# Kernel tuning notes

Hardware: AMD Instinct MI355X
Metric: run time of the kernel (lower is better)

The kernel has to match this reference:

```python
import jax, jax.numpy as jnp
import numpy as np

W_MAE, W_GRAD, W_TV, W_BG, W_MSE = 1.0, 0.1, 0.002, 0.15, 1.0
EPS = 1e-8


def setup_inputs() -> dict:
    key = jax.random.key(0)
    k1, k2, k3 = jax.random.split(key, 3)
    B, C, D, H, W = 2, 3, 128, 128, 128
    pred = jax.random.normal(k1, (B, C, D, H, W), dtype=jnp.float32)
    target = jax.random.normal(k2, (B, C, D, H, W), dtype=jnp.float32)
    # binary foreground mask, broadcast over channels
    mask = (jax.random.uniform(k3, (B, 1, D, H, W)) > 0.5).astype(jnp.float32)
    return {"pred": pred, "target": target, "mask": mask}


def _grad3(x):
    dx = x[:, :, 1:, :, :] - x[:, :, :-1, :, :]
    dy = x[:, :, :, 1:, :] - x[:, :, :, :-1, :]
    dz = x[:, :, :, :, 1:] - x[:, :, :, :, :-1]
    return dx, dy, dz


def reference(pred, target, mask):
    C = pred.shape[1]

    def masked_mean(x, m):
        return (x * m).sum() / (m.sum() * C + EPS)

    pred_in = pred * mask
    tgt_in = target * mask
    diff = pred_in - tgt_in

    l_mae = masked_mean(jnp.abs(diff), mask)

    px, py, pz = _grad3(pred_in)
    tx, ty, tz = _grad3(tgt_in)
    mx = jnp.minimum(mask[:, :, 1:, :, :], mask[:, :, :-1, :, :])
    my = jnp.minimum(mask[:, :, :, 1:, :], mask[:, :, :, :-1, :])
    mz = jnp.minimum(mask[:, :, :, :, 1:], mask[:, :, :, :, :-1])

    l_grad = (masked_mean(jnp.abs(px - tx), mx)
              + masked_mean(jnp.abs(py - ty), my)
              + masked_mean(jnp.abs(pz - tz), mz))
    l_tv = (masked_mean(jnp.abs(px), mx)
            + masked_mean(jnp.abs(py), my)
            + masked_mean(jnp.abs(pz), mz))

    inv = 1.0 - mask
    l_bg = (jnp.abs(pred) * inv).sum() / (inv.sum() * C + EPS)

    l_mse = masked_mean(diff ** 2, mask)

    return (W_MAE * l_mae + W_GRAD * l_grad + W_TV * l_tv
            + W_BG * l_bg + W_MSE * l_mse)
```

## Files before the change

### kernel.cpp

```cpp
#include <hip/hip_runtime.h>

#define NACC 13
#define NPAD 16
#define NBLOCKS 4096
#define NROWS 16384
#define NMID 64

__device__ __forceinline__ float4 ld4(const float* p) {
    return *reinterpret_cast<const float4*>(p);
}

__global__ __launch_bounds__(256) void loss_main(
    const float* __restrict__ pred, const float* __restrict__ target,
    const float* __restrict__ mask, float* __restrict__ partials)
{
    float acc[NACC];
#pragma unroll
    for (int k = 0; k < NACC; ++k) acc[k] = 0.f;

    const int g  = blockIdx.x * 256 + threadIdx.x;
    const int w4 = g & 31;
    const int h  = (g >> 5) & 127;
    const int d  = (g >> 12) & 127;
    const int b  = g >> 19;
    const int w  = w4 << 2;
    const int mb  = b * 2097152 + d * 16384 + h * 128 + w;
    const int pb0 = b * 6291456 + d * 16384 + h * 128 + w;

    const float wv = (w4 < 31) ? 1.f : 0.f;
    const float hv = (h < 127) ? 1.f : 0.f;
    const float dv = (d < 127) ? 1.f : 0.f;
    const int oh = (h < 127) ? 128   : 0;
    const int od = (d < 127) ? 16384 : 0;

    const float4 m0  = ld4(mask + mb);
    const float4 mh  = ld4(mask + mb + oh);
    const float4 md  = ld4(mask + mb + od);
    const float  m4w = __shfl_down(m0.x, 1, 64);

    const float mz0 = fminf(m0.x, m0.y), mz1 = fminf(m0.y, m0.z),
                mz2 = fminf(m0.z, m0.w), mz3 = fminf(m0.w, m4w) * wv;
    const float my0 = fminf(m0.x, mh.x) * hv, my1 = fminf(m0.y, mh.y) * hv,
                my2 = fminf(m0.z, mh.z) * hv, my3 = fminf(m0.w, mh.w) * hv;
    const float mx0 = fminf(m0.x, md.x) * dv, mx1 = fminf(m0.y, md.y) * dv,
                mx2 = fminf(m0.z, md.z) * dv, mx3 = fminf(m0.w, md.w) * dv;

    acc[0] = m0.x + m0.y + m0.z + m0.w;
    acc[1] = mx0 + mx1 + mx2 + mx3;
    acc[2] = my0 + my1 + my2 + my3;
    acc[3] = mz0 + mz1 + mz2 + mz3;

#pragma unroll
    for (int c = 0; c < 3; ++c) {
        const int pb = pb0 + c * 2097152;
        const float4 p0 = ld4(pred + pb);
        const float4 t0 = ld4(target + pb);
        const float4 ph = ld4(pred + pb + oh);
        const float4 th = ld4(target + pb + oh);
        const float4 pd = ld4(pred + pb + od);
        const float4 td = ld4(target + pb + od);
        const float  p4 = __shfl_down(p0.x, 1, 64);
        const float  t4 = __shfl_down(t0.x, 1, 64);

        const float e0x = p0.x - t0.x, e0y = p0.y - t0.y,
                    e0z = p0.z - t0.z, e0w = p0.w - t0.w;
        const float e4  = p4 - t4;

        acc[4] += fabsf(e0x)*m0.x + fabsf(e0y)*m0.y
                + fabsf(e0z)*m0.z + fabsf(e0w)*m0.w;
        acc[5] += e0x*e0x*m0.x + e0y*e0y*m0.y
                + e0z*e0z*m0.z + e0w*e0w*m0.w;
        acc[6] += fabsf(p0.x)*(1.f-m0.x) + fabsf(p0.y)*(1.f-m0.y)
                + fabsf(p0.z)*(1.f-m0.z) + fabsf(p0.w)*(1.f-m0.w);

        acc[9]  += fabsf(e0y-e0x)*mz0 + fabsf(e0z-e0y)*mz1
                 + fabsf(e0w-e0z)*mz2 + fabsf(e4 -e0w)*mz3;
        acc[12] += fabsf(p0.y-p0.x)*mz0 + fabsf(p0.z-p0.y)*mz1
                 + fabsf(p0.w-p0.z)*mz2 + fabsf(p4  -p0.w)*mz3;

        acc[8]  += fabsf((ph.x-th.x)-e0x)*my0 + fabsf((ph.y-th.y)-e0y)*my1
                 + fabsf((ph.z-th.z)-e0z)*my2 + fabsf((ph.w-th.w)-e0w)*my3;
        acc[11] += fabsf(ph.x-p0.x)*my0 + fabsf(ph.y-p0.y)*my1
                 + fabsf(ph.z-p0.z)*my2 + fabsf(ph.w-p0.w)*my3;

        acc[7]  += fabsf((pd.x-td.x)-e0x)*mx0 + fabsf((pd.y-td.y)-e0y)*mx1
                 + fabsf((pd.z-td.z)-e0z)*mx2 + fabsf((pd.w-td.w)-e0w)*mx3;
        acc[10] += fabsf(pd.x-p0.x)*mx0 + fabsf(pd.y-p0.y)*mx1
                 + fabsf(pd.z-p0.z)*mx2 + fabsf(pd.w-p0.w)*mx3;
    }

    const int lane = threadIdx.x & 63;
    const int wave = threadIdx.x >> 6;
    float mine = 0.f;
#pragma unroll
    for (int k = 0; k < NACC; ++k) {
        float v = acc[k];
        for (int o = 32; o > 0; o >>= 1) v += __shfl_down(v, o, 64);
        const float tot = __shfl(v, 0, 64);
        if (lane == k) mine = tot;
    }
    if (lane < NPAD)
        partials[(blockIdx.x * 4 + wave) * NPAD + lane] = mine;
}

__global__ __launch_bounds__(256) void loss_mid(
    const float* __restrict__ partials, float* __restrict__ mid)
{
    const int r = blockIdx.x * 256 + threadIdx.x;
    const float* row = partials + r * NPAD;
    const float4 r0 = ld4(row);     const float4 r1 = ld4(row + 4);
    const float4 r2 = ld4(row + 8); const float4 r3 = ld4(row + 12);
    float acc[NPAD] = {r0.x, r0.y, r0.z, r0.w, r1.x, r1.y, r1.z, r1.w,
                       r2.x, r2.y, r2.z, r2.w, r3.x, r3.y, r3.z, r3.w};

    const int lane = threadIdx.x & 63;
    const int wave = threadIdx.x >> 6;
    __shared__ float red[4][NPAD];
#pragma unroll
    for (int k = 0; k < NPAD; ++k) {
        float v = acc[k];
        for (int o = 32; o > 0; o >>= 1) v += __shfl_down(v, o, 64);
        if (lane == 0) red[wave][k] = v;
    }
    __syncthreads();
    if (threadIdx.x < NPAD) {
        const int k = threadIdx.x;
        mid[blockIdx.x * NPAD + k] =
            red[0][k] + red[1][k] + red[2][k] + red[3][k];
    }
}

__global__ __launch_bounds__(64) void loss_final(
    const float* __restrict__ mid, float* __restrict__ out)
{
    const int lane = threadIdx.x;
    float acc[NPAD];
    {
        const float* row = mid + lane * NPAD;
        const float4 r0 = ld4(row);     const float4 r1 = ld4(row + 4);
        const float4 r2 = ld4(row + 8); const float4 r3 = ld4(row + 12);
        acc[0] = r0.x;  acc[1] = r0.y;  acc[2] = r0.z;  acc[3] = r0.w;
        acc[4] = r1.x;  acc[5] = r1.y;  acc[6] = r1.z;  acc[7] = r1.w;
        acc[8] = r2.x;  acc[9] = r2.y;  acc[10] = r2.z; acc[11] = r2.w;
        acc[12] = r3.x; acc[13] = r3.y; acc[14] = r3.z; acc[15] = r3.w;
    }
#pragma unroll
    for (int k = 0; k < NACC; ++k) {
        for (int o = 32; o > 0; o >>= 1) acc[k] += __shfl_down(acc[k], o, 64);
    }
    if (lane == 0) {
        const float EPS = 1e-8f;
        const float M = acc[0], Mx = acc[1], My = acc[2], Mz = acc[3];
        float loss = (acc[4] + acc[5]) / (3.f * M + EPS);
        loss += 0.1f   * (acc[7] / (3.f*Mx + EPS) + acc[8] / (3.f*My + EPS)
                        + acc[9] / (3.f*Mz + EPS));
        loss += 0.002f * (acc[10] / (3.f*Mx + EPS) + acc[11] / (3.f*My + EPS)
                        + acc[12] / (3.f*Mz + EPS));
        const float inv = 4194304.f - M;
        loss += 0.15f * acc[6] / (3.f * inv + EPS);
        out[0] = loss;
    }
}

extern "C" void kernel_launch(void* const* d_in, const int* in_sizes, int n_in,
                              void* d_out, int out_size, void* d_ws, size_t ws_size,
                              hipStream_t stream) {
    const float* pred   = (const float*)d_in[0];
    const float* target = (const float*)d_in[1];
    const float* mask   = (const float*)d_in[2];
    float* out      = (float*)d_out;
    float* partials = (float*)d_ws;
    float* mid      = partials + NROWS * NPAD;

    loss_main<<<NBLOCKS, 256, 0, stream>>>(pred, target, mask, partials);
    loss_mid<<<NMID, 256, 0, stream>>>(partials, mid);
    loss_final<<<1, 64, 0, stream>>>(mid, out);
}
```

Before: 144.0 us.

## Process four depth slices per thread reusing previous slice for D-gradients

Each thread now walks four consecutive depth planes and keeps the previous plane's pred, target and mask in registers, so the D-direction neighbor no longer needs a separate global load. Only the plane after the chunk is loaded again, at chunk boundaries. The grid shrinks fourfold, and the mid and final reduction kernels are merged into one 1024-thread block that sums the smaller partials array. The cost is more registers per thread and less parallelism in the main kernel.

```diff
diff --git a/kernel.cpp b/kernel.cpp
--- a/kernel.cpp
+++ b/kernel.cpp
@@ -2,15 +2,14 @@
 
 #define NACC 13
 #define NPAD 16
-#define NBLOCKS 4096
-#define NROWS 16384
-#define NMID 64
+#define NBLOCKS 1024
+#define NROWS 4096
 
 __device__ __forceinline__ float4 ld4(const float* p) {
     return *reinterpret_cast<const float4*>(p);
 }
 
-__global__ __launch_bounds__(256) void loss_main(
+__global__ __launch_bounds__(256, 2) void loss_main(
     const float* __restrict__ pred, const float* __restrict__ target,
     const float* __restrict__ mask, float* __restrict__ partials)
 {
@@ -21,72 +20,107 @@
     const int g  = blockIdx.x * 256 + threadIdx.x;
     const int w4 = g & 31;
     const int h  = (g >> 5) & 127;
-    const int d  = (g >> 12) & 127;
-    const int b  = g >> 19;
+    const int dc = (g >> 12) & 31;
+    const int b  = g >> 17;
     const int w  = w4 << 2;
-    const int mb  = b * 2097152 + d * 16384 + h * 128 + w;
-    const int pb0 = b * 6291456 + d * 16384 + h * 128 + w;
+    const int d0 = dc << 2;
 
     const float wv = (w4 < 31) ? 1.f : 0.f;
     const float hv = (h < 127) ? 1.f : 0.f;
-    const float dv = (d < 127) ? 1.f : 0.f;
-    const int oh = (h < 127) ? 128   : 0;
-    const int od = (d < 127) ? 16384 : 0;
-
-    const float4 m0  = ld4(mask + mb);
-    const float4 mh  = ld4(mask + mb + oh);
-    const float4 md  = ld4(mask + mb + od);
-    const float  m4w = __shfl_down(m0.x, 1, 64);
-
-    const float mz0 = fminf(m0.x, m0.y), mz1 = fminf(m0.y, m0.z),
-                mz2 = fminf(m0.z, m0.w), mz3 = fminf(m0.w, m4w) * wv;
-    const float my0 = fminf(m0.x, mh.x) * hv, my1 = fminf(m0.y, mh.y) * hv,
-                my2 = fminf(m0.z, mh.z) * hv, my3 = fminf(m0.w, mh.w) * hv;
-    const float mx0 = fminf(m0.x, md.x) * dv, mx1 = fminf(m0.y, md.y) * dv,
-                mx2 = fminf(m0.z, md.z) * dv, mx3 = fminf(m0.w, md.w) * dv;
-
-    acc[0] = m0.x + m0.y + m0.z + m0.w;
-    acc[1] = mx0 + mx1 + mx2 + mx3;
-    acc[2] = my0 + my1 + my2 + my3;
-    acc[3] = mz0 + mz1 + mz2 + mz3;
-
-#pragma unroll
-    for (int c = 0; c < 3; ++c) {
-        const int pb = pb0 + c * 2097152;
-        const float4 p0 = ld4(pred + pb);
-        const float4 t0 = ld4(target + pb);
-        const float4 ph = ld4(pred + pb + oh);
-        const float4 th = ld4(target + pb + oh);
-        const float4 pd = ld4(pred + pb + od);
-        const float4 td = ld4(target + pb + od);
-        const float  p4 = __shfl_down(p0.x, 1, 64);
-        const float  t4 = __shfl_down(t0.x, 1, 64);
-
-        const float e0x = p0.x - t0.x, e0y = p0.y - t0.y,
-                    e0z = p0.z - t0.z, e0w = p0.w - t0.w;
-        const float e4  = p4 - t4;
-
-        acc[4] += fabsf(e0x)*m0.x + fabsf(e0y)*m0.y
-                + fabsf(e0z)*m0.z + fabsf(e0w)*m0.w;
-        acc[5] += e0x*e0x*m0.x + e0y*e0y*m0.y
-                + e0z*e0z*m0.z + e0w*e0w*m0.w;
-        acc[6] += fabsf(p0.x)*(1.f-m0.x) + fabsf(p0.y)*(1.f-m0.y)
-                + fabsf(p0.z)*(1.f-m0.z) + fabsf(p0.w)*(1.f-m0.w);
-
-        acc[9]  += fabsf(e0y-e0x)*mz0 + fabsf(e0z-e0y)*mz1
-                 + fabsf(e0w-e0z)*mz2 + fabsf(e4 -e0w)*mz3;
-        acc[12] += fabsf(p0.y-p0.x)*mz0 + fabsf(p0.z-p0.y)*mz1
-                 + fabsf(p0.w-p0.z)*mz2 + fabsf(p4  -p0.w)*mz3;
-
-        acc[8]  += fabsf((ph.x-th.x)-e0x)*my0 + fabsf((ph.y-th.y)-e0y)*my1
-                 + fabsf((ph.z-th.z)-e0z)*my2 + fabsf((ph.w-th.w)-e0w)*my3;
-        acc[11] += fabsf(ph.x-p0.x)*my0 + fabsf(ph.y-p0.y)*my1
-                 + fabsf(ph.z-p0.z)*my2 + fabsf(ph.w-p0.w)*my3;
-
-        acc[7]  += fabsf((pd.x-td.x)-e0x)*mx0 + fabsf((pd.y-td.y)-e0y)*mx1
-                 + fabsf((pd.z-td.z)-e0z)*mx2 + fabsf((pd.w-td.w)-e0w)*mx3;
-        acc[10] += fabsf(pd.x-p0.x)*mx0 + fabsf(pd.y-p0.y)*mx1
-                 + fabsf(pd.z-p0.z)*mx2 + fabsf(pd.w-p0.w)*mx3;
+    const int   oh = (h < 127) ? 128 : 0;
+
+    const int mb0 = b * 2097152 + d0 * 16384 + h * 128 + w;
+    const int pb0 = b * 6291456 + d0 * 16384 + h * 128 + w;
+
+    float4 pm;
+    float4 pp[3], pt[3];
+
+#pragma unroll
+    for (int j = 0; j < 4; ++j) {
+        const int mb = mb0 + j * 16384;
+        const float4 m0  = ld4(mask + mb);
+        const float4 mh  = ld4(mask + mb + oh);
+        const float  m4w = __shfl_down(m0.x, 1, 64);
+
+        const float mz0 = fminf(m0.x, m0.y), mz1 = fminf(m0.y, m0.z),
+                    mz2 = fminf(m0.z, m0.w), mz3 = fminf(m0.w, m4w) * wv;
+        const float my0 = fminf(m0.x, mh.x) * hv, my1 = fminf(m0.y, mh.y) * hv,
+                    my2 = fminf(m0.z, mh.z) * hv, my3 = fminf(m0.w, mh.w) * hv;
+
+        acc[0] += m0.x + m0.y + m0.z + m0.w;
+        acc[2] += my0 + my1 + my2 + my3;
+        acc[3] += mz0 + mz1 + mz2 + mz3;
+
+        float mx0 = 0.f, mx1 = 0.f, mx2 = 0.f, mx3 = 0.f;
+        if (j > 0) {
+            mx0 = fminf(pm.x, m0.x); mx1 = fminf(pm.y, m0.y);
+            mx2 = fminf(pm.z, m0.z); mx3 = fminf(pm.w, m0.w);
+            acc[1] += mx0 + mx1 + mx2 + mx3;
+        }
+
+#pragma unroll
+        for (int c = 0; c < 3; ++c) {
+            const int pb = pb0 + j * 16384 + c * 2097152;
+            const float4 p0 = ld4(pred + pb);
+            const float4 t0 = ld4(target + pb);
+            const float4 ph = ld4(pred + pb + oh);
+            const float4 th = ld4(target + pb + oh);
+            const float  p4 = __shfl_down(p0.x, 1, 64);
+            const float  t4 = __shfl_down(t0.x, 1, 64);
+
+            const float e0x = p0.x - t0.x, e0y = p0.y - t0.y,
+                        e0z = p0.z - t0.z, e0w = p0.w - t0.w;
+            const float e4  = p4 - t4;
+
+            acc[4] += fabsf(e0x)*m0.x + fabsf(e0y)*m0.y
+                    + fabsf(e0z)*m0.z + fabsf(e0w)*m0.w;
+            acc[5] += e0x*e0x*m0.x + e0y*e0y*m0.y
+                    + e0z*e0z*m0.z + e0w*e0w*m0.w;
+            acc[6] += fabsf(p0.x)*(1.f-m0.x) + fabsf(p0.y)*(1.f-m0.y)
+                    + fabsf(p0.z)*(1.f-m0.z) + fabsf(p0.w)*(1.f-m0.w);
+
+            acc[9]  += fabsf(e0y-e0x)*mz0 + fabsf(e0z-e0y)*mz1
+                     + fabsf(e0w-e0z)*mz2 + fabsf(e4 -e0w)*mz3;
+            acc[12] += fabsf(p0.y-p0.x)*mz0 + fabsf(p0.z-p0.y)*mz1
+                     + fabsf(p0.w-p0.z)*mz2 + fabsf(p4  -p0.w)*mz3;
+
+            acc[8]  += fabsf((ph.x-th.x)-e0x)*my0 + fabsf((ph.y-th.y)-e0y)*my1
+                     + fabsf((ph.z-th.z)-e0z)*my2 + fabsf((ph.w-th.w)-e0w)*my3;
+            acc[11] += fabsf(ph.x-p0.x)*my0 + fabsf(ph.y-p0.y)*my1
+                     + fabsf(ph.z-p0.z)*my2 + fabsf(ph.w-p0.w)*my3;
+
+            if (j > 0) {
+                const float qx = pp[c].x - pt[c].x, qy = pp[c].y - pt[c].y,
+                            qz = pp[c].z - pt[c].z, qw = pp[c].w - pt[c].w;
+                acc[7]  += fabsf(e0x-qx)*mx0 + fabsf(e0y-qy)*mx1
+                         + fabsf(e0z-qz)*mx2 + fabsf(e0w-qw)*mx3;
+                acc[10] += fabsf(p0.x-pp[c].x)*mx0 + fabsf(p0.y-pp[c].y)*mx1
+                         + fabsf(p0.z-pp[c].z)*mx2 + fabsf(p0.w-pp[c].w)*mx3;
+            }
+            pp[c] = p0; pt[c] = t0;
+        }
+        pm = m0;
+    }
+
+    if (dc < 31) {
+        const float4 mN = ld4(mask + mb0 + 4 * 16384);
+        const float mx0 = fminf(pm.x, mN.x), mx1 = fminf(pm.y, mN.y),
+                    mx2 = fminf(pm.z, mN.z), mx3 = fminf(pm.w, mN.w);
+        acc[1] += mx0 + mx1 + mx2 + mx3;
+#pragma unroll
+        for (int c = 0; c < 3; ++c) {
+            const int pb = pb0 + 4 * 16384 + c * 2097152;
+            const float4 pN = ld4(pred + pb);
+            const float4 tN = ld4(target + pb);
+            const float qx = pp[c].x - pt[c].x, qy = pp[c].y - pt[c].y,
+                        qz = pp[c].z - pt[c].z, qw = pp[c].w - pt[c].w;
+            const float nx = pN.x - tN.x, ny = pN.y - tN.y,
+                        nz = pN.z - tN.z, nw = pN.w - tN.w;
+            acc[7]  += fabsf(nx-qx)*mx0 + fabsf(ny-qy)*mx1
+                     + fabsf(nz-qz)*mx2 + fabsf(nw-qw)*mx3;
+            acc[10] += fabsf(pN.x-pp[c].x)*mx0 + fabsf(pN.y-pp[c].y)*mx1
+                     + fabsf(pN.z-pp[c].z)*mx2 + fabsf(pN.w-pp[c].w)*mx3;
+        }
     }
 
     const int lane = threadIdx.x & 63;
@@ -103,61 +137,54 @@
         partials[(blockIdx.x * 4 + wave) * NPAD + lane] = mine;
 }
 
-__global__ __launch_bounds__(256) void loss_mid(
-    const float* __restrict__ partials, float* __restrict__ mid)
+__global__ __launch_bounds__(1024) void loss_reduce(
+    const float* __restrict__ partials, float* __restrict__ out)
 {
-    const int r = blockIdx.x * 256 + threadIdx.x;
-    const float* row = partials + r * NPAD;
-    const float4 r0 = ld4(row);     const float4 r1 = ld4(row + 4);
-    const float4 r2 = ld4(row + 8); const float4 r3 = ld4(row + 12);
-    float acc[NPAD] = {r0.x, r0.y, r0.z, r0.w, r1.x, r1.y, r1.z, r1.w,
-                       r2.x, r2.y, r2.z, r2.w, r3.x, r3.y, r3.z, r3.w};
-
-    const int lane = threadIdx.x & 63;
-    const int wave = threadIdx.x >> 6;
-    __shared__ float red[4][NPAD];
-#pragma unroll
-    for (int k = 0; k < NPAD; ++k) {
+    const int t    = threadIdx.x;
+    const int lane = t & 63;
+    const int wave = t >> 6;
+
+    float acc[NPAD];
+#pragma unroll
+    for (int k = 0; k < NPAD; ++k) acc[k] = 0.f;
+
+#pragma unroll
+    for (int r = 0; r < 4; ++r) {
+        const float* row = partials + (r * 1024 + t) * NPAD;
+        const float4 r0 = ld4(row);      const float4 r1 = ld4(row + 4);
+        const float4 r2 = ld4(row + 8);  const float4 r3 = ld4(row + 12);
+        acc[0]  += r0.x; acc[1]  += r0.y; acc[2]  += r0.z; acc[3]  += r0.w;
+        acc[4]  += r1.x; acc[5]  += r1.y; acc[6]  += r1.z; acc[7]  += r1.w;
+        acc[8]  += r2.x; acc[9]  += r2.y; acc[10] += r2.z; acc[11] += r2.w;
+        acc[12] += r3.x; acc[13] += r3.y; acc[14] += r3.z; acc[15] += r3.w;
+    }
+
+    __shared__ float red[16][NPAD];
+#pragma unroll
+    for (int k = 0; k < NACC; ++k) {
         float v = acc[k];
         for (int o = 32; o > 0; o >>= 1) v += __shfl_down(v, o, 64);
         if (lane == 0) red[wave][k] = v;
     }
     __syncthreads();
-    if (threadIdx.x < NPAD) {
-        const int k = threadIdx.x;
-        mid[blockIdx.x * NPAD + k] =
-            red[0][k] + red[1][k] + red[2][k] + red[3][k];
-    }
-}
-
-__global__ __launch_bounds__(64) void loss_final(
-    const float* __restrict__ mid, float* __restrict__ out)
-{
-    const int lane = threadIdx.x;
-    float acc[NPAD];
-    {
-        const float* row = mid + lane * NPAD;
-        const float4 r0 = ld4(row);     const float4 r1 = ld4(row + 4);
-        const float4 r2 = ld4(row + 8); const float4 r3 = ld4(row + 12);
-        acc[0] = r0.x;  acc[1] = r0.y;  acc[2] = r0.z;  acc[3] = r0.w;
-        acc[4] = r1.x;  acc[5] = r1.y;  acc[6] = r1.z;  acc[7] = r1.w;
-        acc[8] = r2.x;  acc[9] = r2.y;  acc[10] = r2.z; acc[11] = r2.w;
-        acc[12] = r3.x; acc[13] = r3.y; acc[14] = r3.z; acc[15] = r3.w;
-    }
-#pragma unroll
-    for (int k = 0; k < NACC; ++k) {
-        for (int o = 32; o > 0; o >>= 1) acc[k] += __shfl_down(acc[k], o, 64);
-    }
-    if (lane == 0) {
+
+    if (t == 0) {
+        float tot[NACC];
+#pragma unroll
+        for (int k = 0; k < NACC; ++k) {
+            float s = 0.f;
+            for (int wv2 = 0; wv2 < 16; ++wv2) s += red[wv2][k];
+            tot[k] = s;
+        }
         const float EPS = 1e-8f;
-        const float M = acc[0], Mx = acc[1], My = acc[2], Mz = acc[3];
-        float loss = (acc[4] + acc[5]) / (3.f * M + EPS);
-        loss += 0.1f   * (acc[7] / (3.f*Mx + EPS) + acc[8] / (3.f*My + EPS)
-                        + acc[9] / (3.f*Mz + EPS));
-        loss += 0.002f * (acc[10] / (3.f*Mx + EPS) + acc[11] / (3.f*My + EPS)
-                        + acc[12] / (3.f*Mz + EPS));
+        const float M = tot[0], Mx = tot[1], My = tot[2], Mz = tot[3];
+        float loss = (tot[4] + tot[5]) / (3.f * M + EPS);
+        loss += 0.1f   * (tot[7] / (3.f*Mx + EPS) + tot[8] / (3.f*My + EPS)
+                        + tot[9] / (3.f*Mz + EPS));
+        loss += 0.002f * (tot[10] / (3.f*Mx + EPS) + tot[11] / (3.f*My + EPS)
+                        + tot[12] / (3.f*Mz + EPS));
         const float inv = 4194304.f - M;
-        loss += 0.15f * acc[6] / (3.f * inv + EPS);
+        loss += 0.15f * tot[6] / (3.f * inv + EPS);
         out[0] = loss;
     }
 }
@@ -170,9 +197,7 @@
     const float* mask   = (const float*)d_in[2];
     float* out      = (float*)d_out;
     float* partials = (float*)d_ws;
-    float* mid      = partials + NROWS * NPAD;
 
     loss_main<<<NBLOCKS, 256, 0, stream>>>(pred, target, mask, partials);
-    loss_mid<<<NMID, 256, 0, stream>>>(partials, mid);
-    loss_final<<<1, 64, 0, stream>>>(mid, out);
-}
+    loss_reduce<<<1, 1024, 0, stream>>>(partials, out);
+}
```

Result: slower. 221.8 us (+54.0%).
